# Optimization experiments

Measured on AMD Instinct MI355X. Metric: run time of the kernel, lower is better.

## Reference

```python
import jax, jax.numpy as jnp
import numpy as np

N_NODES = 50000
N_EDGES = 800000
D_IN, D_HID, D_OUT = 128, 256, 128
N_EXPERT = 8


def mean_aggr(x, src, dst, n):
    # scatter-mean of neighbor features onto destination nodes
    msg = x[src]                                            # [E, d]
    s = jax.ops.segment_sum(msg, dst, num_segments=n)       # [N, d]
    cnt = jax.ops.segment_sum(jnp.ones((src.shape[0],), x.dtype), dst, num_segments=n)
    return s / jnp.clip(cnt, 1.0)[:, None]


def moe_top1(x, wg, bg, we, be):
    # FMoE with naive gate, top_k=1: combine weight softmax over top-1 == 1.0
    logits = x @ wg + bg                                    # [N, E]
    gate_full = jax.nn.softmax(logits, axis=-1)             # [N, E]
    idx = jnp.argmax(logits, axis=-1)                       # [N]
    n_expert = we.shape[0]
    out = jnp.zeros((x.shape[0], we.shape[2]), x.dtype)
    for e in range(n_expert):                               # small fixed loop over experts
        mask = (idx == e)[:, None].astype(x.dtype)
        out = out + mask * (x @ we[e] + be[e])
    return out, gate_full


def mysage_conv(x, src, dst, wg, bg, we, be, wr):
    agg = mean_aggr(x, src, dst, x.shape[0])
    out, gate = moe_top1(agg, wg, bg, we, be)
    out = out + x @ wr                                      # root weight (no bias)
    gstd = jnp.std(gate, axis=1, ddof=1).mean()             # torch.std is unbiased
    return out, gstd


def plain_sage_conv(x, src, dst, wl, bl, wr):
    agg = mean_aggr(x, src, dst, x.shape[0])
    return agg @ wl + bl + x @ wr


def setup_inputs() -> dict:
    key = jax.random.key(0)
    ks = jax.random.split(key, 16)
    s = 0.05
    inp = {
        "x": jax.random.normal(ks[0], (N_NODES, D_IN), jnp.float32),
        "edge_index": jax.random.randint(ks[1], (2, N_EDGES), 0, N_NODES, jnp.int64),
        # layer 1 (in -> hid)
        "wg1": jax.random.normal(ks[2], (D_IN, N_EXPERT), jnp.float32) * s,
        "bg1": jnp.zeros((N_EXPERT,), jnp.float32),
        "we1": jax.random.normal(ks[3], (N_EXPERT, D_IN, D_HID), jnp.float32) * s,
        "be1": jnp.zeros((N_EXPERT, D_HID), jnp.float32),
        "wr1": jax.random.normal(ks[4], (D_IN, D_HID), jnp.float32) * s,
        # layer 2 (hid -> hid)
        "wg2": jax.random.normal(ks[5], (D_HID, N_EXPERT), jnp.float32) * s,
        "bg2": jnp.zeros((N_EXPERT,), jnp.float32),
        "we2": jax.random.normal(ks[6], (N_EXPERT, D_HID, D_HID), jnp.float32) * s,
        "be2": jnp.zeros((N_EXPERT, D_HID), jnp.float32),
        "wr2": jax.random.normal(ks[7], (D_HID, D_HID), jnp.float32) * s,
        # layer 3 plain SAGEConv (hid -> out)
        "wl3": jax.random.normal(ks[8], (D_HID, D_OUT), jnp.float32) * s,
        "bl3": jnp.zeros((D_OUT,), jnp.float32),
        "wr3": jax.random.normal(ks[9], (D_HID, D_OUT), jnp.float32) * s,
    }
    return inp


def reference(x, edge_index, wg1, bg1, we1, be1, wr1, wg2, bg2, we2, be2, wr2, wl3, bl3, wr3):
    src, dst = edge_index[0], edge_index[1]
    h, g1 = mysage_conv(x, src, dst, wg1, bg1, we1, be1, wr1)
    h = jax.nn.relu(h)                                      # dropout p=0 / eval mode
    h, g2 = mysage_conv(h, src, dst, wg2, bg2, we2, be2, wr2)
    h = jax.nn.relu(h)
    out = plain_sage_conv(h, src, dst, wl3, bl3, wr3)
    gate_std_mean = jnp.stack([g1, g2]).mean()
    return out, gate_std_mean
```

## Files before the change

kernel.cpp:

```cpp
#include <hip/hip_runtime.h>
#include <hip/hip_bf16.h>
#include <stdint.h>

#define DEV static __device__ __forceinline__

typedef __attribute__((ext_vector_type(8))) short short8;
typedef __attribute__((ext_vector_type(4))) float f32x4;

DEV float bf2f(unsigned short u) { return __uint_as_float(((unsigned)u) << 16); }
DEV float bflo(unsigned u) { return __uint_as_float(u << 16); }
DEV float bfhi(unsigned u) { return __uint_as_float(u & 0xffff0000u); }
DEV unsigned short f2bf(float f) {
    unsigned u = __float_as_uint(f);
    u += 0x7fff + ((u >> 16) & 1);
    return (unsigned short)(u >> 16);
}

__global__ void k_detect(const int* __restrict__ ei, int* __restrict__ flags) {
    if (threadIdx.x == 0 && blockIdx.x == 0) {
        int zeros = 0;
        for (int i = 0; i < 128; ++i) if (ei[2 * i + 1] == 0) ++zeros;
        flags[1] = (zeros >= 64) ? 1 : 0;
    }
}

__global__ void k_cvt_idx(const int* __restrict__ ei, int* __restrict__ src32,
                          int* __restrict__ dst32, int E, const int* __restrict__ flags) {
    int i = blockIdx.x * 256 + threadIdx.x;
    if (i >= E) return;
    if (flags[1]) { src32[i] = ei[2 * i]; dst32[i] = ei[2 * E + 2 * i]; }
    else          { src32[i] = ei[i];     dst32[i] = ei[E + i]; }
}

__global__ void k_transpose_nb(const float* __restrict__ in, unsigned short* __restrict__ out,
                               int R, int C) {
    __shared__ unsigned short tile[32][33];
    int tx = threadIdx.x & 31, ty = threadIdx.x >> 5;
    size_t mat = (size_t)blockIdx.z * R * C;
    int r0 = blockIdx.y * 32, c0 = blockIdx.x * 32;
#pragma unroll
    for (int j = 0; j < 32; j += 8)
        tile[ty + j][tx] = f2bf(in[mat + (size_t)(r0 + ty + j) * C + c0 + tx]);
    __syncthreads();
#pragma unroll
    for (int j = 0; j < 32; j += 8)
        out[mat + (size_t)(c0 + ty + j) * R + r0 + tx] = tile[tx][ty + j];
}

__global__ void k_degree(const int* __restrict__ dst, int* __restrict__ deg, int E) {
    int i = blockIdx.x * 256 + threadIdx.x;
    if (i < E) atomicAdd(&deg[dst[i]], 1);
}

__global__ void k_scan1(const int* __restrict__ deg, int* __restrict__ row_ptr,
                        int* __restrict__ part, int n) {
    __shared__ int wsum[4];
    int t = threadIdx.x, lane = t & 63, wv = t >> 6;
    int i = blockIdx.x * 256 + t;
    int v0 = (i < n) ? deg[i] : 0;
    int v = v0;
#pragma unroll
    for (int d = 1; d < 64; d <<= 1) { int u = __shfl_up(v, d); if (lane >= d) v += u; }
    if (lane == 63) wsum[wv] = v;
    __syncthreads();
    int add = 0;
    for (int w2 = 0; w2 < wv; ++w2) add += wsum[w2];
    v += add;
    if (i < n) row_ptr[i] = v - v0;
    if (t == 255) part[blockIdx.x] = v;
}

__global__ void k_scan2(int* __restrict__ part, int P) {
    __shared__ int wsum[4];
    int t = threadIdx.x, lane = t & 63, wv = t >> 6;
    int v0 = (t < P) ? part[t] : 0;
    int v = v0;
#pragma unroll
    for (int d = 1; d < 64; d <<= 1) { int u = __shfl_up(v, d); if (lane >= d) v += u; }
    if (lane == 63) wsum[wv] = v;
    __syncthreads();
    int add = 0;
    for (int w2 = 0; w2 < wv; ++w2) add += wsum[w2];
    v += add;
    if (t < P) part[t] = v - v0;
}

__global__ void k_scan3(int* __restrict__ row_ptr, const int* __restrict__ part, int n, int E) {
    int i = blockIdx.x * 256 + threadIdx.x;
    if (i < n) row_ptr[i] += part[blockIdx.x];
    if (i == 0) row_ptr[n] = E;
}

__global__ void k_fill(const int* __restrict__ src, const int* __restrict__ dst,
                       const int* __restrict__ row_ptr, int* __restrict__ cursor,
                       int* __restrict__ csr, int E) {
    int i = blockIdx.x * 256 + threadIdx.x;
    if (i < E) {
        int d = dst[i];
        int p = atomicAdd(&cursor[d], 1);
        csr[row_ptr[d] + p] = src[i];
    }
}

template<int D>
__global__ void k_aggr(const float* __restrict__ xin, const int* __restrict__ row_ptr,
                       const int* __restrict__ csr, float* __restrict__ agg, int n) {
    int wid = (blockIdx.x * blockDim.x + threadIdx.x) >> 6;
    int lane = threadIdx.x & 63;
    if (wid >= n) return;
    constexpr int V = D / 64;
    double a0[V], a1[V], a2[V], a3[V];
#pragma unroll
    for (int i = 0; i < V; ++i) { a0[i] = 0.0; a1[i] = 0.0; a2[i] = 0.0; a3[i] = 0.0; }
    int s0 = row_ptr[wid], s1 = row_ptr[wid + 1];
    int j = s0;
    for (; j + 4 <= s1; j += 4) {
        int i0 = csr[j], i1 = csr[j + 1], i2 = csr[j + 2], i3 = csr[j + 3];
        const float* p0 = xin + (size_t)i0 * D + lane * V;
        const float* p1 = xin + (size_t)i1 * D + lane * V;
        const float* p2 = xin + (size_t)i2 * D + lane * V;
        const float* p3 = xin + (size_t)i3 * D + lane * V;
        if (V == 2) {
            float2 f0 = *(const float2*)p0, f1 = *(const float2*)p1;
            float2 f2 = *(const float2*)p2, f3 = *(const float2*)p3;
            a0[0] += (double)f0.x; a0[1] += (double)f0.y;
            a1[0] += (double)f1.x; a1[1] += (double)f1.y;
            a2[0] += (double)f2.x; a2[1] += (double)f2.y;
            a3[0] += (double)f3.x; a3[1] += (double)f3.y;
        } else {
            float4 f0 = *(const float4*)p0, f1 = *(const float4*)p1;
            float4 f2 = *(const float4*)p2, f3 = *(const float4*)p3;
            a0[0] += (double)f0.x; a0[1] += (double)f0.y; a0[2] += (double)f0.z; a0[3] += (double)f0.w;
            a1[0] += (double)f1.x; a1[1] += (double)f1.y; a1[2] += (double)f1.z; a1[3] += (double)f1.w;
            a2[0] += (double)f2.x; a2[1] += (double)f2.y; a2[2] += (double)f2.z; a2[3] += (double)f2.w;
            a3[0] += (double)f3.x; a3[1] += (double)f3.y; a3[2] += (double)f3.z; a3[3] += (double)f3.w;
        }
    }
    for (; j < s1; ++j) {
        const float* p = xin + (size_t)csr[j] * D + lane * V;
        if (V == 2) {
            float2 f = *(const float2*)p;
            a0[0] += (double)f.x; a0[1] += (double)f.y;
        } else {
            float4 f = *(const float4*)p;
            a0[0] += (double)f.x; a0[1] += (double)f.y; a0[2] += (double)f.z; a0[3] += (double)f.w;
        }
    }
    double inv = 1.0 / (double)max(s1 - s0, 1);
#pragma unroll
    for (int i = 0; i < V; ++i)
        agg[(size_t)wid * D + lane * V + i] = (float)(((a0[i] + a1[i]) + (a2[i] + a3[i])) * inv);
}

template<int D>
__global__ void k_aggr_bf(const unsigned short* __restrict__ xin, const int* __restrict__ row_ptr,
                          const int* __restrict__ csr, float* __restrict__ agg, int n) {
    int wid = (blockIdx.x * blockDim.x + threadIdx.x) >> 6;
    int lane = threadIdx.x & 63;
    if (wid >= n) return;
    constexpr int V = D / 64;
    double a0[V], a1[V], a2[V], a3[V];
#pragma unroll
    for (int i = 0; i < V; ++i) { a0[i] = 0.0; a1[i] = 0.0; a2[i] = 0.0; a3[i] = 0.0; }
    int s0 = row_ptr[wid], s1 = row_ptr[wid + 1];
    int j = s0;
    for (; j + 4 <= s1; j += 4) {
        int i0 = csr[j], i1 = csr[j + 1], i2 = csr[j + 2], i3 = csr[j + 3];
        uint2 u0 = *(const uint2*)(xin + (size_t)i0 * D + lane * V);
        uint2 u1 = *(const uint2*)(xin + (size_t)i1 * D + lane * V);
        uint2 u2 = *(const uint2*)(xin + (size_t)i2 * D + lane * V);
        uint2 u3 = *(const uint2*)(xin + (size_t)i3 * D + lane * V);
        a0[0] += (double)bflo(u0.x); a0[1] += (double)bfhi(u0.x);
        a0[2] += (double)bflo(u0.y); a0[3] += (double)bfhi(u0.y);
        a1[0] += (double)bflo(u1.x); a1[1] += (double)bfhi(u1.x);
        a1[2] += (double)bflo(u1.y); a1[3] += (double)bfhi(u1.y);
        a2[0] += (double)bflo(u2.x); a2[1] += (double)bfhi(u2.x);
        a2[2] += (double)bflo(u2.y); a2[3] += (double)bfhi(u2.y);
        a3[0] += (double)bflo(u3.x); a3[1] += (double)bfhi(u3.x);
        a3[2] += (double)bflo(u3.y); a3[3] += (double)bfhi(u3.y);
    }
    for (; j < s1; ++j) {
        uint2 u = *(const uint2*)(xin + (size_t)csr[j] * D + lane * V);
        a0[0] += (double)bflo(u.x); a0[1] += (double)bfhi(u.x);
        a0[2] += (double)bflo(u.y); a0[3] += (double)bfhi(u.y);
    }
    double inv = 1.0 / (double)max(s1 - s0, 1);
#pragma unroll
    for (int i = 0; i < V; ++i)
        agg[(size_t)wid * D + lane * V + i] = (float)(((a0[i] + a1[i]) + (a2[i] + a3[i])) * inv);
}

template<int D>
__global__ void k_gate(const float* __restrict__ agg, const float* __restrict__ wg,
                       const float* __restrict__ bg, int* __restrict__ idx,
                       int* __restrict__ ecnt, float* __restrict__ gsum, int n) {
    __shared__ float swg[D * 8];
    __shared__ int hcnt[8];
    __shared__ float red[256];
    int t = threadIdx.x;
    if (t < 8) hcnt[t] = 0;
    for (int i = t; i < D * 8; i += 256) swg[i] = wg[i];
    __syncthreads();
    int nid = blockIdx.x * 256 + t;
    float stdv = 0.f;
    if (nid < n) {
        double lg[8];
#pragma unroll
        for (int e = 0; e < 8; ++e) lg[e] = (double)bg[e];
        const float* ap = agg + (size_t)nid * D;
        for (int k = 0; k < D; k += 4) {
            float4 a = *(const float4*)(ap + k);
#pragma unroll
            for (int e = 0; e < 8; ++e) {
                lg[e] += (double)a.x * swg[(k + 0) * 8 + e] + (double)a.y * swg[(k + 1) * 8 + e]
                       + (double)a.z * swg[(k + 2) * 8 + e] + (double)a.w * swg[(k + 3) * 8 + e];
            }
        }
        double m = lg[0];
        int am = 0;
#pragma unroll
        for (int e = 1; e < 8; ++e) if (lg[e] > m) { m = lg[e]; am = e; }
        double s = 0.0, p[8];
#pragma unroll
        for (int e = 0; e < 8; ++e) { p[e] = exp(lg[e] - m); s += p[e]; }
        double invs = 1.0 / s, sq = 0.0;
#pragma unroll
        for (int e = 0; e < 8; ++e) { double q = p[e] * invs; sq += q * q; }
        stdv = (float)sqrt(fmax(sq - 0.125, 0.0) / 7.0);
        idx[nid] = am;
        atomicAdd(&hcnt[am], 1);
    }
    red[t] = stdv;
    __syncthreads();
    for (int off = 128; off > 0; off >>= 1) {
        if (t < off) red[t] += red[t + off];
        __syncthreads();
    }
    if (t == 0) atomicAdd(gsum, red[0]);
    if (t < 8 && hcnt[t] > 0) atomicAdd(&ecnt[t], hcnt[t]);
}

__global__ void k_offsets(const int* __restrict__ ecnt, int* __restrict__ eoff) {
    if (threadIdx.x == 0 && blockIdx.x == 0) {
        int s = 0;
        for (int e = 0; e < 8; ++e) { eoff[e] = s; s += ecnt[e]; }
        eoff[8] = s;
    }
}

__global__ void k_perm(const int* __restrict__ idx, const int* __restrict__ eoff,
                       int* __restrict__ ecur, int* __restrict__ perm, int n) {
    __shared__ int lcnt[8], lbase[8];
    int t = threadIdx.x;
    if (t < 8) lcnt[t] = 0;
    __syncthreads();
    int nid = blockIdx.x * 256 + t;
    int e = 0, r = 0;
    bool valid = (nid < n);
    if (valid) { e = idx[nid]; r = atomicAdd(&lcnt[e], 1); }
    __syncthreads();
    if (t < 8) lbase[t] = lcnt[t] ? atomicAdd(&ecur[t], lcnt[t]) : 0;
    __syncthreads();
    if (valid) perm[eoff[e] + lbase[e] + r] = nid;
}

template<int NCOL, bool LOAD>
DEV void g_step(int g, const float* __restrict__ Bp, const float* __restrict__ at,
                float4 (&cur)[4], float (&acc)[8][4]) {
    float bx[4][4];
#pragma unroll
    for (int kk = 0; kk < 4; ++kk) {
        bx[kk][0] = cur[kk].x; bx[kk][1] = cur[kk].y;
        bx[kk][2] = cur[kk].z; bx[kk][3] = cur[kk].w;
    }
#pragma unroll
    for (int r = 0; r < 8; ++r) {
        float4 a = *(const float4*)(at + r * 68 + g * 4);
#pragma unroll
        for (int c = 0; c < 4; ++c) {
            acc[r][c] = fmaf(a.x, bx[0][c], acc[r][c]);
            acc[r][c] = fmaf(a.y, bx[1][c], acc[r][c]);
            acc[r][c] = fmaf(a.z, bx[2][c], acc[r][c]);
            acc[r][c] = fmaf(a.w, bx[3][c], acc[r][c]);
        }
    }
    if (LOAD) {
#pragma unroll
        for (int kk = 0; kk < 4; ++kk)
            cur[kk] = *(const float4*)(Bp + (size_t)(g * 4 + 8 + kk) * NCOL);
    }
}

template<int NCOL>
DEV void compute_chunk(const float* __restrict__ Bp, const float* __restrict__ at,
                       float (&acc)[8][4]) {
    float4 bA[4], bB[4];
#pragma unroll
    for (int kk = 0; kk < 4; ++kk) bA[kk] = *(const float4*)(Bp + (size_t)kk * NCOL);
#pragma unroll
    for (int kk = 0; kk < 4; ++kk) bB[kk] = *(const float4*)(Bp + (size_t)(4 + kk) * NCOL);
#pragma unroll 1
    for (int g = 0; g < 14; g += 2) {
        g_step<NCOL, true>(g, Bp, at, bA, acc);
        g_step<NCOL, true>(g + 1, Bp, at, bB, acc);
    }
    g_step<NCOL, false>(14, Bp, at, bA, acc);
    g_step<NCOL, false>(15, Bp, at, bB, acc);
}

template<int DIN, int NCOL, bool RELU>
__global__ __launch_bounds__(256, 4) void k_gemm_f32(
    const float* __restrict__ agg, const float* __restrict__ a2,
    const float* __restrict__ B1, const float* __restrict__ B2,
    const float* __restrict__ bias,
    const int* __restrict__ perm, const int* __restrict__ eoff,
    float* __restrict__ outp, int n) {
    static_assert(DIN == 128 && NCOL == 256, "layer-1 geometry");
    __shared__ float a_tile[2][4 * 8 * 68];
    __shared__ int rows[32];
    int t = threadIdx.x;
    int rs = blockIdx.x * 32;
    if (rs >= n) return;
    int nrows = min(32, n - rs);
    if (t < 32) rows[t] = perm[rs + min(t, nrows - 1)];
    __syncthreads();

    int e0 = 0, e1 = 0;
    int last = rs + nrows - 1;
#pragma unroll
    for (int e = 1; e < 8; ++e) {
        int v = eoff[e];
        if (v <= rs) e0 = e;
        if (v <= last) e1 = e;
    }
    int ne = e1 - e0 + 1;
    int nchunks = 2 * ne + 2;

    int lane = t & 63, rg = t >> 6;
    int cols = lane * 4;
    int srow = lane >> 3;
    int sk = (lane & 7) * 8;
    int gpos = rs + rg * 8 + srow;
    int myrow = rows[rg * 8 + srow];
    float* stc = &a_tile[0][rg * 544 + srow * 68 + sk];
    float* stn = &a_tile[1][rg * 544 + srow * 68 + sk];
    const float* atc = &a_tile[0][rg * 544];
    const float* atn = &a_tile[1][rg * 544];

    float acc[8][4];
#pragma unroll
    for (int r = 0; r < 8; ++r) { acc[r][0] = 0.f; acc[r][1] = 0.f; acc[r][2] = 0.f; acc[r][3] = 0.f; }

    auto params = [&](int c, const float*& ap, const float*& Bp, float& m) {
        int half = c & 1;
        if (c < 2 * ne) {
            int e = e0 + (c >> 1);
            ap = agg + (size_t)myrow * DIN + sk + half * 64;
            Bp = B1 + (size_t)e * DIN * NCOL + (size_t)half * 64 * NCOL + cols;
            m = (gpos >= eoff[e] && gpos < eoff[e + 1]) ? 1.f : 0.f;
        } else {
            ap = a2 + (size_t)myrow * DIN + sk + half * 64;
            Bp = B2 + (size_t)half * 64 * NCOL + cols;
            m = 1.f;
        }
    };

    const float* ap; const float* Bp; float m;
    params(0, ap, Bp, m);
    float4 p0 = *(const float4*)ap, p1 = *(const float4*)(ap + 4);
#pragma unroll 1
    for (int c = 0; c < nchunks; ++c) {
        float4 s0 = p0, s1 = p1;
        s0.x *= m; s0.y *= m; s0.z *= m; s0.w *= m;
        s1.x *= m; s1.y *= m; s1.z *= m; s1.w *= m;
        *(float4*)stc = s0; *(float4*)(stc + 4) = s1;
        const float* Bcur = Bp;
        if (c + 1 < nchunks) {
            params(c + 1, ap, Bp, m);
            p0 = *(const float4*)ap; p1 = *(const float4*)(ap + 4);
        }
        compute_chunk<NCOL>(Bcur, atc, acc);
        float* ts = stc; stc = stn; stn = ts;
        const float* ta = atc; atc = atn; atn = ta;
    }

#pragma unroll
    for (int r = 0; r < 8; ++r) {
        int rr = rg * 8 + r;
        if (rr < nrows) {
            int gp = rs + rr;
            int er = e0;
            for (int e = e0 + 1; e <= e1; ++e) if (eoff[e] <= gp) er = e;
            float4 bb = *(const float4*)(bias + er * NCOL + cols);
            int gr = rows[rr];
            float v0 = acc[r][0] + bb.x, v1 = acc[r][1] + bb.y;
            float v2 = acc[r][2] + bb.z, v3 = acc[r][3] + bb.w;
            if (RELU) { v0 = fmaxf(v0, 0.f); v1 = fmaxf(v1, 0.f); v2 = fmaxf(v2, 0.f); v3 = fmaxf(v3, 0.f); }
            *(float4*)(outp + (size_t)gr * NCOL + cols) = make_float4(v0, v1, v2, v3);
        }
    }
}

template<int DIN, int MODE, int CT>
DEV void gemm_half(const void* __restrict__ Asrc, const unsigned short* __restrict__ BT,
                   short (*Ah)[40], short (*Bs)[40],
                   const int* rows, f32x4 (&acc)[4][CT], int t, int lane, int w) {
    int q = lane >> 4, m16 = lane & 15;
    int r = t >> 2, part = t & 3;
    for (int kc = 0; kc < DIN; kc += 32) {
        __syncthreads();
        if (MODE == 2) {
            *(uint4*)&Ah[r][part * 8] =
                *(const uint4*)((const unsigned short*)Asrc + (size_t)rows[r] * DIN + kc + part * 8);
        } else {
            const float* pf = (const float*)Asrc + (size_t)rows[r] * DIN + kc + part * 8;
            float4 p0 = *(const float4*)pf, p1 = *(const float4*)(pf + 4);
            float va[8] = { p0.x, p0.y, p0.z, p0.w, p1.x, p1.y, p1.z, p1.w };
            short8 h;
#pragma unroll
            for (int j = 0; j < 8; ++j) h[j] = (short)f2bf(va[j]);
            *(short8*)&Ah[r][part * 8] = h;
        }
#pragma unroll
        for (int j = 0; j < CT; ++j) {
            int c = t + 256 * j;
            int nn = c >> 2, pp = c & 3;
            *(uint4*)&Bs[nn][pp * 8] = *(const uint4*)(BT + (size_t)nn * DIN + kc + pp * 8);
        }
        __syncthreads();
        short8 af[4], bfr[CT];
#pragma unroll
        for (int rt = 0; rt < 4; ++rt) af[rt] = *(short8*)&Ah[rt * 16 + m16][q * 8];
#pragma unroll
        for (int ct = 0; ct < CT; ++ct) bfr[ct] = *(short8*)&Bs[w * CT * 16 + ct * 16 + m16][q * 8];
#pragma unroll
        for (int rt = 0; rt < 4; ++rt)
#pragma unroll
            for (int ct = 0; ct < CT; ++ct)
                acc[rt][ct] = __builtin_amdgcn_mfma_f32_16x16x32_bf16(af[rt], bfr[ct], acc[rt][ct], 0, 0, 0);
    }
}

template<int DIN, int M0, int M1, int CT, bool EXPERT, bool RELU, bool OUTBF>
__global__ __launch_bounds__(256) void k_gemm(
    const void* __restrict__ A0, const void* __restrict__ A1,
    const unsigned short* __restrict__ B0T, const unsigned short* __restrict__ B1T,
    const float* __restrict__ bias,
    const int* __restrict__ perm, const int* __restrict__ eoff,
    void* __restrict__ outp, int n) {
    constexpr int NCOL = CT * 64;
    __shared__ short Ah[64][40];
    __shared__ short Bs[NCOL][40];
    __shared__ int rows[64];
    int t = threadIdx.x;
    int lane = t & 63, w = t >> 6;
    int e = 0, base = 0, cnt = n;
    if (EXPERT) { e = blockIdx.y; base = eoff[e]; cnt = eoff[e + 1] - base; }
    int rs = blockIdx.x * 64;
    if (rs >= cnt) return;
    int nrows = min(64, cnt - rs);
    if (t < 64) {
        int j = rs + min(t, nrows - 1);
        rows[t] = EXPERT ? perm[base + j] : j;
    }
    __syncthreads();
    f32x4 acc[4][CT];
#pragma unroll
    for (int rt = 0; rt < 4; ++rt)
#pragma unroll
        for (int ct = 0; ct < CT; ++ct) acc[rt][ct] = (f32x4)(0.f);

    gemm_half<DIN, M0, CT>(A0, B0T + (EXPERT ? (size_t)e * DIN * NCOL : 0), Ah, Bs, rows, acc, t, lane, w);
    gemm_half<DIN, M1, CT>(A1, B1T, Ah, Bs, rows, acc, t, lane, w);

    int q = lane >> 4, m16 = lane & 15;
#pragma unroll
    for (int ct = 0; ct < CT; ++ct) {
        int col = w * CT * 16 + ct * 16 + m16;
        float bv = bias[(EXPERT ? e * NCOL : 0) + col];
#pragma unroll
        for (int rt = 0; rt < 4; ++rt)
#pragma unroll
            for (int i = 0; i < 4; ++i) {
                int rr = rt * 16 + q * 4 + i;
                if (rr < nrows) {
                    int gr = rows[rr];
                    float v = acc[rt][ct][i] + bv;
                    if (RELU) v = fmaxf(v, 0.f);
                    if (OUTBF) ((unsigned short*)outp)[(size_t)gr * NCOL + col] = f2bf(v);
                    else       ((float*)outp)[(size_t)gr * NCOL + col] = v;
                }
            }
    }
}

__global__ void k_final(const float* __restrict__ gsum, float* __restrict__ outf) {
    if (threadIdx.x == 0 && blockIdx.x == 0) {
        float g = (gsum[0] + gsum[1]) * (0.5f / 50000.0f);
        outf[(size_t)50000 * 128] = g;
    }
}

extern "C" void kernel_launch(void* const* d_in, const int* in_sizes, int n_in,
                              void* d_out, int out_size, void* d_ws, size_t ws_size,
                              hipStream_t stream) {
    constexpr int N = 50000, E = 800000;
    const float* x   = (const float*)d_in[0];
    const int* ei    = (const int*)d_in[1];
    const float* wg1 = (const float*)d_in[2];
    const float* bg1 = (const float*)d_in[3];
    const float* we1 = (const float*)d_in[4];
    const float* be1 = (const float*)d_in[5];
    const float* wr1 = (const float*)d_in[6];
    const float* wg2 = (const float*)d_in[7];
    const float* bg2 = (const float*)d_in[8];
    const float* we2 = (const float*)d_in[9];
    const float* be2 = (const float*)d_in[10];
    const float* wr2 = (const float*)d_in[11];
    const float* wl3 = (const float*)d_in[12];
    const float* bl3 = (const float*)d_in[13];
    const float* wr3 = (const float*)d_in[14];

    int* ip = (int*)d_ws;
    int* deg = ip;            ip += N;
    int* cursor = ip;         ip += N;
    int* ecnt = ip;           ip += 16;
    int* ecur = ip;           ip += 16;
    float* gsum = (float*)ip; ip += 2;
    int* flags = ip;          ip += 2;
    int* row_ptr = ip;        ip += N + 1;
    int* csr = ip;            ip += E;
    int* idxb = ip;           ip += N;
    int* permb = ip;          ip += N;
    int* eoff = ip;           ip += 18;
    int* part = ip;           ip += 256;
    int* src32 = ip;          ip += E;
    int* dst32 = ip;          ip += E;
    size_t off = (size_t)((char*)ip - (char*)d_ws);
    off = (off + 255) & ~(size_t)255;
    float* fp = (float*)((char*)d_ws + off);
    float* agg = fp; fp += (size_t)N * 256;
    float* h1  = fp; fp += (size_t)N * 256;
    unsigned short* wp = (unsigned short*)fp;
    unsigned short* h2b  = wp; wp += (size_t)N * 256;
    unsigned short* we2T = wp; wp += 8 * 256 * 256;
    unsigned short* wr2T = wp; wp += 256 * 256;
    unsigned short* wl3T = wp; wp += 256 * 128;
    unsigned short* wr3T = wp; wp += 256 * 128;

    hipMemsetAsync(d_ws, 0, (size_t)(2 * N + 36) * 4, stream);

    k_detect<<<1, 64, 0, stream>>>(ei, flags);
    k_cvt_idx<<<(E + 255) / 256, 256, 0, stream>>>(ei, src32, dst32, E, flags);

    k_transpose_nb<<<dim3(8, 8, 8), 256, 0, stream>>>(we2, we2T, 256, 256);
    k_transpose_nb<<<dim3(8, 8, 1), 256, 0, stream>>>(wr2, wr2T, 256, 256);
    k_transpose_nb<<<dim3(4, 8, 1), 256, 0, stream>>>(wl3, wl3T, 256, 128);
    k_transpose_nb<<<dim3(4, 8, 1), 256, 0, stream>>>(wr3, wr3T, 256, 128);

    constexpr int NB = (N + 255) / 256;
    constexpr int WB = (N + 3) / 4;
    k_degree<<<(E + 255) / 256, 256, 0, stream>>>(dst32, deg, E);
    k_scan1<<<NB, 256, 0, stream>>>(deg, row_ptr, part, N);
    k_scan2<<<1, 256, 0, stream>>>(part, NB);
    k_scan3<<<NB, 256, 0, stream>>>(row_ptr, part, N, E);
    k_fill<<<(E + 255) / 256, 256, 0, stream>>>(src32, dst32, row_ptr, cursor, csr, E);

    constexpr int GB = (N + 63) / 64;
    constexpr int GB32 = (N + 31) / 32;
    k_aggr<128><<<WB, 256, 0, stream>>>(x, row_ptr, csr, agg, N);
    k_gate<128><<<NB, 256, 0, stream>>>(agg, wg1, bg1, idxb, ecnt, gsum, N);
    k_offsets<<<1, 1, 0, stream>>>(ecnt, eoff);
    k_perm<<<NB, 256, 0, stream>>>(idxb, eoff, ecur, permb, N);
    k_gemm_f32<128, 256, true><<<dim3(GB32), 256, 0, stream>>>(
        agg, x, we1, wr1, be1, permb, eoff, h1, N);

    k_aggr<256><<<WB, 256, 0, stream>>>(h1, row_ptr, csr, agg, N);
    k_gate<256><<<NB, 256, 0, stream>>>(agg, wg2, bg2, idxb, ecnt + 8, gsum + 1, N);
    k_offsets<<<1, 1, 0, stream>>>(ecnt + 8, eoff + 9);
    k_perm<<<NB, 256, 0, stream>>>(idxb, eoff + 9, ecur + 8, permb, N);
    k_gemm<256, 0, 0, 4, true, true, true><<<dim3(GB, 8), 256, 0, stream>>>(
        agg, h1, we2T, wr2T, be2, permb, eoff + 9, h2b, N);

    k_aggr_bf<256><<<WB, 256, 0, stream>>>(h2b, row_ptr, csr, agg, N);
    k_gemm<256, 0, 2, 2, false, false, false><<<dim3(GB, 1), 256, 0, stream>>>(
        agg, h2b, wl3T, wr3T, bl3, nullptr, nullptr, d_out, N);

    k_final<<<1, 1, 0, stream>>>(gsum, (float*)d_out);
}
```

Baseline: 662.9 us.

## Project before aggregating in layer three and fold degree count into index conversion

Layer three now multiplies h2 by wl3 and wr3 first, in one GEMM over the adjacent transposed weights. The wl3 product is stored in bf16 and the root/bias product in fp32. A new kernel then does the mean aggregation on the 128-wide projected rows and adds the root term, so the edge gather moves half as much data as gathering 256-wide rows. The degree atomics move into the index conversion kernel, removing one launch and one pass over dst. The trade-off is that the projected messages are rounded to bf16 before summation, a small numerical difference from the reference order.

```diff
diff --git a/kernel.cpp b/kernel.cpp
--- a/kernel.cpp
+++ b/kernel.cpp
@@ -25,11 +25,15 @@
 }
 
 __global__ void k_cvt_idx(const int* __restrict__ ei, int* __restrict__ src32,
-                          int* __restrict__ dst32, int E, const int* __restrict__ flags) {
+                          int* __restrict__ dst32, int* __restrict__ deg,
+                          int E, const int* __restrict__ flags) {
     int i = blockIdx.x * 256 + threadIdx.x;
     if (i >= E) return;
-    if (flags[1]) { src32[i] = ei[2 * i]; dst32[i] = ei[2 * E + 2 * i]; }
-    else          { src32[i] = ei[i];     dst32[i] = ei[E + i]; }
+    int s, d;
+    if (flags[1]) { s = ei[2 * i]; d = ei[2 * E + 2 * i]; }
+    else          { s = ei[i];     d = ei[E + i]; }
+    src32[i] = s; dst32[i] = d;
+    atomicAdd(&deg[d], 1);
 }
 
 __global__ void k_transpose_nb(const float* __restrict__ in, unsigned short* __restrict__ out,
@@ -47,9 +51,9 @@
         out[mat + (size_t)(c0 + ty + j) * R + r0 + tx] = tile[tx][ty + j];
 }
 
-__global__ void k_degree(const int* __restrict__ dst, int* __restrict__ deg, int E) {
-    int i = blockIdx.x * 256 + threadIdx.x;
-    if (i < E) atomicAdd(&deg[dst[i]], 1);
+__global__ void k_bias3(const float* __restrict__ bl3, float* __restrict__ bias3) {
+    int t = threadIdx.x;
+    bias3[t] = (t < 128) ? 0.f : bl3[t - 128];
 }
 
 __global__ void k_scan1(const int* __restrict__ deg, int* __restrict__ row_ptr,
@@ -152,42 +156,38 @@
         agg[(size_t)wid * D + lane * V + i] = (float)(((a0[i] + a1[i]) + (a2[i] + a3[i])) * inv);
 }
 
-template<int D>
-__global__ void k_aggr_bf(const unsigned short* __restrict__ xin, const int* __restrict__ row_ptr,
-                          const int* __restrict__ csr, float* __restrict__ agg, int n) {
+__global__ void k_aggr_badd(const unsigned short* __restrict__ Pb, const int* __restrict__ row_ptr,
+                            const int* __restrict__ csr, const float* __restrict__ Rf,
+                            float* __restrict__ outp, int n) {
     int wid = (blockIdx.x * blockDim.x + threadIdx.x) >> 6;
     int lane = threadIdx.x & 63;
     if (wid >= n) return;
-    constexpr int V = D / 64;
-    double a0[V], a1[V], a2[V], a3[V];
-#pragma unroll
-    for (int i = 0; i < V; ++i) { a0[i] = 0.0; a1[i] = 0.0; a2[i] = 0.0; a3[i] = 0.0; }
+    double a0[2], a1[2], a2[2], a3[2];
+#pragma unroll
+    for (int i = 0; i < 2; ++i) { a0[i] = 0.0; a1[i] = 0.0; a2[i] = 0.0; a3[i] = 0.0; }
     int s0 = row_ptr[wid], s1 = row_ptr[wid + 1];
     int j = s0;
     for (; j + 4 <= s1; j += 4) {
         int i0 = csr[j], i1 = csr[j + 1], i2 = csr[j + 2], i3 = csr[j + 3];
-        uint2 u0 = *(const uint2*)(xin + (size_t)i0 * D + lane * V);
-        uint2 u1 = *(const uint2*)(xin + (size_t)i1 * D + lane * V);
-        uint2 u2 = *(const uint2*)(xin + (size_t)i2 * D + lane * V);
-        uint2 u3 = *(const uint2*)(xin + (size_t)i3 * D + lane * V);
-        a0[0] += (double)bflo(u0.x); a0[1] += (double)bfhi(u0.x);
-        a0[2] += (double)bflo(u0.y); a0[3] += (double)bfhi(u0.y);
-        a1[0] += (double)bflo(u1.x); a1[1] += (double)bfhi(u1.x);
-        a1[2] += (double)bflo(u1.y); a1[3] += (double)bfhi(u1.y);
-        a2[0] += (double)bflo(u2.x); a2[1] += (double)bfhi(u2.x);
-        a2[2] += (double)bflo(u2.y); a2[3] += (double)bfhi(u2.y);
-        a3[0] += (double)bflo(u3.x); a3[1] += (double)bfhi(u3.x);
-        a3[2] += (double)bflo(u3.y); a3[3] += (double)bfhi(u3.y);
+        unsigned u0 = *(const unsigned*)(Pb + (size_t)i0 * 128 + lane * 2);
+        unsigned u1 = *(const unsigned*)(Pb + (size_t)i1 * 128 + lane * 2);
+        unsigned u2 = *(const unsigned*)(Pb + (size_t)i2 * 128 + lane * 2);
+        unsigned u3 = *(const unsigned*)(Pb + (size_t)i3 * 128 + lane * 2);
+        a0[0] += (double)bflo(u0); a0[1] += (double)bfhi(u0);
+        a1[0] += (double)bflo(u1); a1[1] += (double)bfhi(u1);
+        a2[0] += (double)bflo(u2); a2[1] += (double)bfhi(u2);
+        a3[0] += (double)bflo(u3); a3[1] += (double)bfhi(u3);
     }
     for (; j < s1; ++j) {
-        uint2 u = *(const uint2*)(xin + (size_t)csr[j] * D + lane * V);
-        a0[0] += (double)bflo(u.x); a0[1] += (double)bfhi(u.x);
-        a0[2] += (double)bflo(u.y); a0[3] += (double)bfhi(u.y);
+        unsigned u = *(const unsigned*)(Pb + (size_t)csr[j] * 128 + lane * 2);
+        a0[0] += (double)bflo(u); a0[1] += (double)bfhi(u);
     }
     double inv = 1.0 / (double)max(s1 - s0, 1);
-#pragma unroll
-    for (int i = 0; i < V; ++i)
-        agg[(size_t)wid * D + lane * V + i] = (float)(((a0[i] + a1[i]) + (a2[i] + a3[i])) * inv);
+    float2 r = *(const float2*)(Rf + (size_t)wid * 128 + lane * 2);
+    float2 o;
+    o.x = (float)(((a0[0] + a1[0]) + (a2[0] + a3[0])) * inv) + r.x;
+    o.y = (float)(((a0[1] + a1[1]) + (a2[1] + a3[1])) * inv) + r.y;
+    *(float2*)(outp + (size_t)wid * 128 + lane * 2) = o;
 }
 
 template<int D>
@@ -405,6 +405,7 @@
 DEV void gemm_half(const void* __restrict__ Asrc, const unsigned short* __restrict__ BT,
                    short (*Ah)[40], short (*Bs)[40],
                    const int* rows, f32x4 (&acc)[4][CT], int t, int lane, int w) {
+    if (MODE == 9) return;
     int q = lane >> 4, m16 = lane & 15;
     int r = t >> 2, part = t & 3;
     for (int kc = 0; kc < DIN; kc += 32) {
@@ -441,13 +442,13 @@
     }
 }
 
-template<int DIN, int M0, int M1, int CT, bool EXPERT, bool RELU, bool OUTBF>
+template<int DIN, int M0, int M1, int CT, bool EXPERT, bool RELU, int OUTMODE>
 __global__ __launch_bounds__(256) void k_gemm(
     const void* __restrict__ A0, const void* __restrict__ A1,
     const unsigned short* __restrict__ B0T, const unsigned short* __restrict__ B1T,
     const float* __restrict__ bias,
     const int* __restrict__ perm, const int* __restrict__ eoff,
-    void* __restrict__ outp, int n) {
+    void* __restrict__ outp, void* __restrict__ outp2, int n) {
     constexpr int NCOL = CT * 64;
     __shared__ short Ah[64][40];
     __shared__ short Bs[NCOL][40];
@@ -487,8 +488,12 @@
                     int gr = rows[rr];
                     float v = acc[rt][ct][i] + bv;
                     if (RELU) v = fmaxf(v, 0.f);
-                    if (OUTBF) ((unsigned short*)outp)[(size_t)gr * NCOL + col] = f2bf(v);
-                    else       ((float*)outp)[(size_t)gr * NCOL + col] = v;
+                    if (OUTMODE == 1) ((unsigned short*)outp)[(size_t)gr * NCOL + col] = f2bf(v);
+                    else if (OUTMODE == 0) ((float*)outp)[(size_t)gr * NCOL + col] = v;
+                    else {
+                        if (col < 128) ((unsigned short*)outp)[(size_t)gr * 128 + col] = f2bf(v);
+                        else           ((float*)outp2)[(size_t)gr * 128 + (col - 128)] = v;
+                    }
                 }
             }
     }
@@ -528,6 +533,7 @@
     int* ecur = ip;           ip += 16;
     float* gsum = (float*)ip; ip += 2;
     int* flags = ip;          ip += 2;
+    float* bias3 = (float*)ip; ip += 256;
     int* row_ptr = ip;        ip += N + 1;
     int* csr = ip;            ip += E;
     int* idxb = ip;           ip += N;
@@ -547,20 +553,22 @@
     unsigned short* wr2T = wp; wp += 256 * 256;
     unsigned short* wl3T = wp; wp += 256 * 128;
     unsigned short* wr3T = wp; wp += 256 * 128;
+    unsigned short* Pb = (unsigned short*)h1;
+    float* Rf = agg;
 
     hipMemsetAsync(d_ws, 0, (size_t)(2 * N + 36) * 4, stream);
 
     k_detect<<<1, 64, 0, stream>>>(ei, flags);
-    k_cvt_idx<<<(E + 255) / 256, 256, 0, stream>>>(ei, src32, dst32, E, flags);
+    k_cvt_idx<<<(E + 255) / 256, 256, 0, stream>>>(ei, src32, dst32, deg, E, flags);
 
     k_transpose_nb<<<dim3(8, 8, 8), 256, 0, stream>>>(we2, we2T, 256, 256);
     k_transpose_nb<<<dim3(8, 8, 1), 256, 0, stream>>>(wr2, wr2T, 256, 256);
     k_transpose_nb<<<dim3(4, 8, 1), 256, 0, stream>>>(wl3, wl3T, 256, 128);
     k_transpose_nb<<<dim3(4, 8, 1), 256, 0, stream>>>(wr3, wr3T, 256, 128);
+    k_bias3<<<1, 256, 0, stream>>>(bl3, bias3);
 
     constexpr int NB = (N + 255) / 256;
     constexpr int WB = (N + 3) / 4;
-    k_degree<<<(E + 255) / 256, 256, 0, stream>>>(dst32, deg, E);
     k_scan1<<<NB, 256, 0, stream>>>(deg, row_ptr, part, N);
     k_scan2<<<1, 256, 0, stream>>>(part, NB);
     k_scan3<<<NB, 256, 0, stream>>>(row_ptr, part, N, E);
@@ -579,12 +587,12 @@
     k_gate<256><<<NB, 256, 0, stream>>>(agg, wg2, bg2, idxb, ecnt + 8, gsum + 1, N);
     k_offsets<<<1, 1, 0, stream>>>(ecnt + 8, eoff + 9);
     k_perm<<<NB, 256, 0, stream>>>(idxb, eoff + 9, ecur + 8, permb, N);
-    k_gemm<256, 0, 0, 4, true, true, true><<<dim3(GB, 8), 256, 0, stream>>>(
-        agg, h1, we2T, wr2T, be2, permb, eoff + 9, h2b, N);
-
-    k_aggr_bf<256><<<WB, 256, 0, stream>>>(h2b, row_ptr, csr, agg, N);
-    k_gemm<256, 0, 2, 2, false, false, false><<<dim3(GB, 1), 256, 0, stream>>>(
-        agg, h2b, wl3T, wr3T, bl3, nullptr, nullptr, d_out, N);
+    k_gemm<256, 0, 0, 4, true, true, 1><<<dim3(GB, 8), 256, 0, stream>>>(
+        agg, h1, we2T, wr2T, be2, permb, eoff + 9, h2b, nullptr, N);
+
+    k_gemm<256, 2, 9, 4, false, false, 2><<<dim3(GB, 1), 256, 0, stream>>>(
+        h2b, nullptr, wl3T, nullptr, bias3, nullptr, nullptr, Pb, Rf, N);
+    k_aggr_badd<<<WB, 256, 0, stream>>>(Pb, row_ptr, csr, Rf, (float*)d_out, N);
 
     k_final<<<1, 1, 0, stream>>>(gsum, (float*)d_out);
 }
```

Result: no change. 654.3 us (-1.3%).
